# Optimization experiments

Measured on AMD Instinct MI355X. Metric: run time of the kernel, lower is better.

## Reference

```python
import jax, jax.numpy as jnp
import numpy as np

GRAD_CLIP = 50.0
MIN_DIST = 1e-10


def _logpsi(x_flat, W1, b1, W2, b2, w3):
    # x_flat: [D] flattened electron coordinates -> scalar log|psi|
    h = jnp.tanh(x_flat @ W1 + b1)
    h = jnp.tanh(h @ W2 + b2)
    return h @ w3


def setup_inputs() -> dict:
    key = jax.random.key(0)
    k = jax.random.split(key, 6)
    B, NE, H = 1024, 16, 512
    D = NE * 3
    electron_coords = jax.random.normal(k[0], (B, NE, 3), dtype=jnp.float32)
    atom_coords = jnp.asarray(
        [[0.0, 0.0, 0.0], [1.4, 0.0, 0.0], [0.0, 1.4, 0.0], [0.0, 0.0, 1.4]],
        dtype=jnp.float32)
    nuclear_charges = jnp.ones((4,), dtype=jnp.float32)
    W1 = jax.random.normal(k[1], (D, H), dtype=jnp.float32) / np.float32(np.sqrt(D))
    b1 = jnp.zeros((H,), dtype=jnp.float32)
    W2 = jax.random.normal(k[2], (H, H), dtype=jnp.float32) / np.float32(np.sqrt(H))
    b2 = jnp.zeros((H,), dtype=jnp.float32)
    w3 = jax.random.normal(k[3], (H,), dtype=jnp.float32) / np.float32(np.sqrt(H))
    return {"electron_coords": electron_coords, "atom_coords": atom_coords,
            "nuclear_charges": nuclear_charges,
            "W1": W1, "b1": b1, "W2": W2, "b2": b2, "w3": w3}


def _kinetic_log(electron_coords, W1, b1, W2, b2, w3):
    # kinetic = -0.5 * (lap log psi + |grad log psi|^2), per batch element
    B, NE, _ = electron_coords.shape
    D = NE * 3
    x = electron_coords.reshape(B, D)

    def f(xi):
        return _logpsi(xi, W1, b1, W2, b2, w3)

    def per_sample(xi):
        g = jax.grad(f)(xi)                       # [D]
        hdiag = jnp.diagonal(jax.jacfwd(jax.grad(f))(xi))  # [D]
        return g, hdiag

    g, hdiag = jax.vmap(per_sample)(x)            # [B, D] each
    hdiag = jnp.where(jnp.isfinite(hdiag),
                      jnp.clip(hdiag, -GRAD_CLIP, GRAD_CLIP), 0.0)
    lap = hdiag.sum(-1)
    gsq = (g ** 2).sum(-1)
    return jnp.clip(-0.5 * (lap + gsq), -100.0, 100.0)


def _potential(electron_coords, atom_coords, nuclear_charges):
    B, NE, _ = electron_coords.shape
    NA = atom_coords.shape[0]
    # electron-electron repulsion, sum over i<j
    d_ee = electron_coords[:, :, None, :] - electron_coords[:, None, :, :]
    r_ee = jnp.sqrt((d_ee ** 2).sum(-1) + jnp.eye(NE, dtype=electron_coords.dtype))
    r_ee = jnp.maximum(r_ee, MIN_DIST)
    iu = jnp.triu(jnp.ones((NE, NE), dtype=bool), 1)
    e_e = jnp.where(iu, 1.0 / r_ee, 0.0).sum((1, 2))
    # electron-nucleus attraction
    d_en = electron_coords[:, :, None, :] - atom_coords[None, None, :, :]
    r_en = jnp.maximum(jnp.sqrt((d_en ** 2).sum(-1)), MIN_DIST)  # [B, NE, NA]
    e_n = -(nuclear_charges[None, None, :] / r_en).sum((1, 2))
    # nucleus-nucleus repulsion (constant over batch)
    d_nn = atom_coords[:, None, :] - atom_coords[None, :, :]
    r_nn = jnp.sqrt((d_nn ** 2).sum(-1) + jnp.eye(NA, dtype=atom_coords.dtype))
    iun = jnp.triu(jnp.ones((NA, NA), dtype=bool), 1)
    zz = nuclear_charges[:, None] * nuclear_charges[None, :]
    n_n = jnp.where(iun & (r_nn > MIN_DIST), zz / r_nn, 0.0).sum()
    return jnp.clip(e_e + e_n + n_n, -1000.0, 1000.0)


def reference(electron_coords, atom_coords, nuclear_charges, W1, b1, W2, b2, w3):
    kinetic = _kinetic_log(electron_coords, W1, b1, W2, b2, w3)
    potential = _potential(electron_coords, atom_coords, nuclear_charges)
    return kinetic + potential
```

## Files before the change

kernel.cpp:

```cpp
#include <hip/hip_runtime.h>
#include <math.h>

#define BTOT 1024
#define NE   16
#define NA   4
#define DD   48
#define HH   512
#define ROWS (BTOT * DD)

#define GBM 128
#define GBN 128
#define GBK 64
#define NCB (HH / GBN)
#define MG  (NCB * (ROWS / GBM))
#define NU  128
#define NT  (HH / GBK)

typedef __attribute__((ext_vector_type(8))) short bf16x8;
typedef __attribute__((ext_vector_type(8))) unsigned short u16x8;
typedef __attribute__((ext_vector_type(4))) float f32x4;

__device__ inline unsigned short f2bf(float f) {
  unsigned int u = __builtin_bit_cast(unsigned int, f);
  u += 0x7fffu + ((u >> 16) & 1u);
  return (unsigned short)(u >> 16);
}
__device__ inline float bf2f(unsigned short s) {
  unsigned int u = ((unsigned int)s) << 16;
  return __builtin_bit_cast(float, u);
}

__device__ inline int swz(int row, int chunk) {
  return (row << 6) + ((chunk ^ (row & 7)) << 3);
}

__device__ inline void gload16(const ushort* g, ushort* l) {
  __builtin_amdgcn_global_load_lds(
      (const __attribute__((address_space(1))) unsigned int*)g,
      (__attribute__((address_space(3))) unsigned int*)l, 16, 0, 0);
}

__device__ inline void gemm128_k_loop(const ushort* __restrict__ abase,
                                      const ushort* __restrict__ bbase,
                                      ushort* As, ushort* Bs,
                                      int w, int l, f32x4 acc[4][4]) {
  const int lrow = l >> 3;
  const int cg = (l & 7) ^ lrow;
  const ushort* __restrict__ ap = abase + (w * 32 + lrow) * HH + cg * 8;
  const ushort* __restrict__ bp = bbase + (w * 32 + lrow) * HH + cg * 8;
  const int wm = w >> 1, wn = w & 1;
  const int lr = l & 15, lg = l >> 4;

#pragma unroll
  for (int q = 0; q < 4; ++q) {
    gload16(ap + q * 8 * HH, As + (w * 4 + q) * 512);
    gload16(bp + q * 8 * HH, Bs + (w * 4 + q) * 512);
  }
  __syncthreads();

  for (int kt = 0; kt < NT; ++kt) {
    const int cur = (kt & 1) << 13;
    if (kt + 1 < NT) {
      const int nxt = ((kt + 1) & 1) << 13;
      const int koff = (kt + 1) * GBK;
#pragma unroll
      for (int q = 0; q < 4; ++q) {
        gload16(ap + koff + q * 8 * HH, As + nxt + (w * 4 + q) * 512);
        gload16(bp + koff + q * 8 * HH, Bs + nxt + (w * 4 + q) * 512);
      }
    }
#pragma unroll
    for (int k0 = 0; k0 < GBK; k0 += 32) {
      const int ck = (k0 >> 3) + lg;
      bf16x8 af[4], bfr[4];
#pragma unroll
      for (int m = 0; m < 4; ++m)
        af[m] = *reinterpret_cast<const bf16x8*>(
            &As[cur + swz(wm * 64 + m * 16 + lr, ck)]);
#pragma unroll
      for (int n = 0; n < 4; ++n)
        bfr[n] = *reinterpret_cast<const bf16x8*>(
            &Bs[cur + swz(wn * 64 + n * 16 + lr, ck)]);
#pragma unroll
      for (int m = 0; m < 4; ++m)
#pragma unroll
        for (int n = 0; n < 4; ++n)
          acc[m][n] = __builtin_amdgcn_mfma_f32_16x16x32_bf16(af[m], bfr[n],
                                                              acc[m][n], 0, 0, 0);
    }
    __syncthreads();
  }
}

__device__ inline void gemm64_k_loop(const ushort* __restrict__ abase,
                                     const ushort* __restrict__ bbase,
                                     ushort* As, ushort* Bs,
                                     int w, int l, f32x4 acc[2][2]) {
  const int lrow = l >> 3;
  const int cg = (l & 7) ^ lrow;
  const ushort* __restrict__ ap = abase + (w * 16 + lrow) * HH + cg * 8;
  const ushort* __restrict__ bp = bbase + (w * 16 + lrow) * HH + cg * 8;
  const int wm = w >> 1, wn = w & 1;
  const int lr = l & 15, lg = l >> 4;

#pragma unroll
  for (int q = 0; q < 2; ++q) {
    gload16(ap + q * 8 * HH, As + (w * 2 + q) * 512);
    gload16(bp + q * 8 * HH, Bs + (w * 2 + q) * 512);
  }
  __syncthreads();

  for (int kt = 0; kt < NT; ++kt) {
    const int cur = (kt & 1) << 12;
    if (kt + 1 < NT) {
      const int nxt = ((kt + 1) & 1) << 12;
      const int koff = (kt + 1) * GBK;
#pragma unroll
      for (int q = 0; q < 2; ++q) {
        gload16(ap + koff + q * 8 * HH, As + nxt + (w * 2 + q) * 512);
        gload16(bp + koff + q * 8 * HH, Bs + nxt + (w * 2 + q) * 512);
      }
    }
#pragma unroll
    for (int k0 = 0; k0 < GBK; k0 += 32) {
      const int ck = (k0 >> 3) + lg;
      bf16x8 af[2], bfr[2];
#pragma unroll
      for (int m = 0; m < 2; ++m)
        af[m] = *reinterpret_cast<const bf16x8*>(
            &As[cur + swz(wm * 32 + m * 16 + lr, ck)]);
#pragma unroll
      for (int n = 0; n < 2; ++n)
        bfr[n] = *reinterpret_cast<const bf16x8*>(
            &Bs[cur + swz(wn * 32 + n * 16 + lr, ck)]);
#pragma unroll
      for (int m = 0; m < 2; ++m)
#pragma unroll
        for (int n = 0; n < 2; ++n)
          acc[m][n] = __builtin_amdgcn_mfma_f32_16x16x32_bf16(af[m], bfr[n],
                                                              acc[m][n], 0, 0, 0);
    }
    __syncthreads();
  }
}

__global__ __launch_bounds__(256) void k_l1pot(
    const float* __restrict__ X, const float* __restrict__ ATOM,
    const float* __restrict__ Z, const float* __restrict__ W1,
    const float* __restrict__ B1, const float* __restrict__ W2,
    ushort* __restrict__ W2b, ushort* __restrict__ W2Tb,
    ushort* __restrict__ T1b, float* __restrict__ D1,
    ushort* __restrict__ Ab, float* __restrict__ POT) {
  const int b = blockIdx.x, tid = threadIdx.x;
  __shared__ float xs[DD];
  __shared__ float d1s[HH];
  __shared__ float red[256];
  __shared__ float tile[32][33];

  if (b < 256) {
    const int bx = (b & 15) * 32, by = (b >> 4) * 32;
    const int tx = tid & 31, ty = tid >> 5;
    for (int r = 0; r < 32; r += 8) {
      float v = W2[(by + ty + r) * HH + bx + tx];
      tile[ty + r][tx] = v;
      W2b[(by + ty + r) * HH + bx + tx] = f2bf(v);
    }
    __syncthreads();
    for (int r = 0; r < 32; r += 8)
      W2Tb[(bx + ty + r) * HH + by + tx] = f2bf(tile[tx][ty + r]);
  }

  if (tid < DD) xs[tid] = X[b * DD + tid];
  __syncthreads();

  {
    const int j0 = tid * 2;
    float acc0 = B1[j0], acc1 = B1[j0 + 1];
#pragma unroll 8
    for (int i = 0; i < DD; ++i) {
      float xv = xs[i];
      float2 w = *reinterpret_cast<const float2*>(&W1[i * HH + j0]);
      acc0 = fmaf(xv, w.x, acc0);
      acc1 = fmaf(xv, w.y, acc1);
    }
    float t0 = tanhf(acc0), t1v = tanhf(acc1);
    unsigned int pk = ((unsigned int)f2bf(t1v) << 16) | f2bf(t0);
    *reinterpret_cast<unsigned int*>(&T1b[b * HH + j0]) = pk;
    float dd0 = 1.f - t0 * t0, dd1 = 1.f - t1v * t1v;
    d1s[j0] = dd0; d1s[j0 + 1] = dd1;
    *reinterpret_cast<float2*>(&D1[b * HH + j0]) = make_float2(dd0, dd1);
  }
  __syncthreads();

  {
    const int k0 = tid * 2;
    const float dd0 = d1s[k0], dd1 = d1s[k0 + 1];
#pragma unroll 4
    for (int i = 0; i < DD; ++i) {
      float2 w = *reinterpret_cast<const float2*>(&W1[i * HH + k0]);
      unsigned int pk =
          ((unsigned int)f2bf(w.y * dd1) << 16) | f2bf(w.x * dd0);
      *reinterpret_cast<unsigned int*>(&Ab[(b * DD + i) * HH + k0]) = pk;
    }
  }

  {
    float p = 0.f;
    for (int pr = tid; pr < NE * (NE - 1) / 2; pr += 256) {
      int i = 0, rem = pr;
      while (rem >= NE - 1 - i) { rem -= NE - 1 - i; ++i; }
      int j = i + 1 + rem;
      float dx = xs[i * 3 + 0] - xs[j * 3 + 0];
      float dy = xs[i * 3 + 1] - xs[j * 3 + 1];
      float dz = xs[i * 3 + 2] - xs[j * 3 + 2];
      float r = fmaxf(sqrtf(dx * dx + dy * dy + dz * dz), 1e-10f);
      p += 1.f / r;
    }
    for (int idx = tid; idx < NE * NA; idx += 256) {
      int e = idx / NA, a = idx % NA;
      float dx = xs[e * 3 + 0] - ATOM[a * 3 + 0];
      float dy = xs[e * 3 + 1] - ATOM[a * 3 + 1];
      float dz = xs[e * 3 + 2] - ATOM[a * 3 + 2];
      float r = fmaxf(sqrtf(dx * dx + dy * dy + dz * dz), 1e-10f);
      p -= Z[a] / r;
    }
    if (tid == 0) {
      for (int a = 0; a < NA; ++a)
        for (int a2 = a + 1; a2 < NA; ++a2) {
          float dx = ATOM[a * 3 + 0] - ATOM[a2 * 3 + 0];
          float dy = ATOM[a * 3 + 1] - ATOM[a2 * 3 + 1];
          float dz = ATOM[a * 3 + 2] - ATOM[a2 * 3 + 2];
          float r = sqrtf(dx * dx + dy * dy + dz * dz);
          if (r > 1e-10f) p += Z[a] * Z[a2] / r;
        }
    }
    red[tid] = p;
    __syncthreads();
    for (int s = 128; s > 0; s >>= 1) {
      if (tid < s) red[tid] += red[tid + s];
      __syncthreads();
    }
    if (tid == 0) POT[b] = fminf(fmaxf(red[0], -1000.f), 1000.f);
  }
}

__global__ __launch_bounds__(256) void k_act64(
    const ushort* __restrict__ Ab, const ushort* __restrict__ Bb,
    const float* __restrict__ B2, const float* __restrict__ w3,
    float* __restrict__ C2, ushort* __restrict__ Vb) {
  const int rb = blockIdx.x >> 3;
  const int cb = blockIdx.x & 7;
  const int row0 = rb * 64, col0 = cb * 64;
  const int t = threadIdx.x, w = t >> 6, l = t & 63;

  __shared__ ushort As[2 * 64 * GBK];
  __shared__ ushort Bs[2 * 64 * GBK];

  f32x4 acc[2][2];
#pragma unroll
  for (int m = 0; m < 2; ++m)
#pragma unroll
    for (int n = 0; n < 2; ++n) acc[m][n] = (f32x4)0.f;

  gemm64_k_loop(Ab + row0 * HH, Bb + col0 * HH, As, Bs, w, l, acc);

  const int wm = w >> 1, wn = w & 1, lr = l & 15, lg = l >> 4;
#pragma unroll
  for (int m = 0; m < 2; ++m)
#pragma unroll
    for (int e = 0; e < 4; ++e) {
      const int row = row0 + wm * 32 + m * 16 + lg * 4 + e;
#pragma unroll
      for (int n = 0; n < 2; ++n) {
        const int col = col0 + wn * 32 + n * 16 + lr;
        float a2 = acc[m][n][e] + B2[col];
        float t2 = tanhf(a2);
        float d2 = 1.f - t2 * t2;
        float w3v = w3[col];
        C2[row * HH + col] = -2.f * t2 * d2 * w3v;
        Vb[row * HH + col] = f2bf(w3v * d2);
      }
    }
}

__global__ __launch_bounds__(256) void k_mu(
    const ushort* __restrict__ Abig, const ushort* __restrict__ W2Tb,
    const float* __restrict__ C2, float* __restrict__ HD2P,
    const ushort* __restrict__ Vb, const ushort* __restrict__ W2b,
    const float* __restrict__ D1, const ushort* __restrict__ T1b,
    float* __restrict__ S1, ushort* __restrict__ C1b) {
  const int t = threadIdx.x, w = t >> 6, l = t & 63;
  __shared__ ushort As[2 * GBM * GBK];
  __shared__ ushort Bs[2 * GBN * GBK];

  if (blockIdx.x < NU) {
    const int ub = blockIdx.x;
    const int rb = ub >> 3, cb = ub & 7;
    const int row0 = rb * 64, col0 = cb * 64;

    f32x4 acc[2][2];
#pragma unroll
    for (int m = 0; m < 2; ++m)
#pragma unroll
      for (int n = 0; n < 2; ++n) acc[m][n] = (f32x4)0.f;

    gemm64_k_loop(Vb + row0 * HH, W2b + col0 * HH, As, Bs, w, l, acc);

    const int wm = w >> 1, wn = w & 1, lr = l & 15, lg = l >> 4;
#pragma unroll
    for (int m = 0; m < 2; ++m)
#pragma unroll
      for (int e = 0; e < 4; ++e) {
        const int row = row0 + wm * 32 + m * 16 + lg * 4 + e;
#pragma unroll
        for (int n = 0; n < 2; ++n) {
          const int col = col0 + wn * 32 + n * 16 + lr;
          float u = acc[m][n][e];
          float d1 = D1[row * HH + col];
          float t1 = bf2f(T1b[row * HH + col]);
          S1[row * HH + col] = d1 * u;
          C1b[row * HH + col] = f2bf(-2.f * t1 * d1 * u);
        }
      }
  } else {
    const int bid = blockIdx.x - NU;
    const int wgid = (bid & 7) * (MG / 8) + (bid >> 3);
    const int cb = wgid & 3;
    const int rb = wgid >> 2;
    const int row0 = rb * GBM, col0 = cb * GBN;

    f32x4 acc[4][4];
#pragma unroll
    for (int m = 0; m < 4; ++m)
#pragma unroll
      for (int n = 0; n < 4; ++n) acc[m][n] = (f32x4)0.f;

    gemm128_k_loop(Abig + row0 * HH, W2Tb + col0 * HH, As, Bs, w, l, acc);

    const int wm = w >> 1, wn = w & 1, lr = l & 15, lg = l >> 4;
#pragma unroll
    for (int m = 0; m < 4; ++m) {
#pragma unroll
      for (int e = 0; e < 4; ++e) {
        const int row_g = row0 + wm * 64 + m * 16 + lg * 4 + e;
        const int bs2 = row_g / DD;
        const float* __restrict__ c2p = &C2[bs2 * HH + col0 + wn * 64 + lr];
        float s = 0.f;
#pragma unroll
        for (int n = 0; n < 4; ++n) {
          float mv = acc[m][n][e];
          s = fmaf(c2p[n * 16] * mv, mv, s);
        }
        s += __shfl_xor(s, 1);
        s += __shfl_xor(s, 2);
        s += __shfl_xor(s, 4);
        s += __shfl_xor(s, 8);
        if (lr == 0) HD2P[cb * ROWS + row_g] = s;
      }
    }
  }
}

__global__ __launch_bounds__(256) void k_grad_fin(
    const float* __restrict__ W1, const float* __restrict__ S1,
    const ushort* __restrict__ C1b, const float* __restrict__ HD2P,
    const float* __restrict__ POT, float* __restrict__ OUT) {
  const int b = blockIdx.x, tid = threadIdx.x;
  __shared__ float gtmp[DD], htmp[DD];
  const int wid = tid >> 6, lane = tid & 63;
  const int j0 = lane * 8;

  for (int i = wid; i < DD; i += 4) {
    float4 wa = *reinterpret_cast<const float4*>(&W1[i * HH + j0]);
    float4 wb = *reinterpret_cast<const float4*>(&W1[i * HH + j0 + 4]);
    float4 sa = *reinterpret_cast<const float4*>(&S1[b * HH + j0]);
    float4 sb = *reinterpret_cast<const float4*>(&S1[b * HH + j0 + 4]);
    u16x8 cv = *reinterpret_cast<const u16x8*>(&C1b[b * HH + j0]);
    float wv[8] = {wa.x, wa.y, wa.z, wa.w, wb.x, wb.y, wb.z, wb.w};
    float sv[8] = {sa.x, sa.y, sa.z, sa.w, sb.x, sb.y, sb.z, sb.w};
    float gp = 0.f, hp = 0.f;
#pragma unroll
    for (int e = 0; e < 8; ++e) {
      gp = fmaf(wv[e], sv[e], gp);
      hp = fmaf(wv[e] * wv[e], bf2f(cv[e]), hp);
    }
#pragma unroll
    for (int off = 32; off > 0; off >>= 1) {
      gp += __shfl_down(gp, off);
      hp += __shfl_down(hp, off);
    }
    if (lane == 0) { gtmp[i] = gp; htmp[i] = hp; }
  }
  __syncthreads();

  if (tid < 64) {
    float gv = 0.f, hv = 0.f;
    if (tid < DD) {
      gv = gtmp[tid];
      float h = htmp[tid];
#pragma unroll
      for (int c = 0; c < NCB; ++c) h += HD2P[c * ROWS + b * DD + tid];
      if (h >= -1e30f && h <= 1e30f) h = fminf(fmaxf(h, -50.f), 50.f);
      else h = 0.f;
      hv = h;
    }
    float sq = gv * gv;
#pragma unroll
    for (int off = 32; off > 0; off >>= 1) {
      sq += __shfl_down(sq, off);
      hv += __shfl_down(hv, off);
    }
    if (tid == 0) {
      float kin = fminf(fmaxf(-0.5f * (hv + sq), -100.f), 100.f);
      OUT[b] = kin + POT[b];
    }
  }
}

extern "C" void kernel_launch(void* const* d_in, const int* in_sizes, int n_in,
                              void* d_out, int out_size, void* d_ws, size_t ws_size,
                              hipStream_t stream) {
  const float* X    = (const float*)d_in[0];
  const float* ATOM = (const float*)d_in[1];
  const float* Z    = (const float*)d_in[2];
  const float* W1   = (const float*)d_in[3];
  const float* B1   = (const float*)d_in[4];
  const float* W2   = (const float*)d_in[5];
  const float* B2   = (const float*)d_in[6];
  const float* w3   = (const float*)d_in[7];
  float* out = (float*)d_out;

  float* ws = (float*)d_ws;
  ushort* W2b  = (ushort*)(ws + 0);
  ushort* W2Tb = (ushort*)(ws + 131072);
  ushort* T1b  = (ushort*)(ws + 262144);
  ushort* Vb   = (ushort*)(ws + 524288);
  ushort* C1b  = (ushort*)(ws + 786432);
  float*  S1   = ws + 1048576;
  float*  D1   = ws + 1572864;
  float*  C2   = ws + 2097152;
  float*  POT  = ws + 2621440;
  float*  HD2P = ws + 2622464;
  ushort* Abig = (ushort*)(ws + 2819072);

  k_l1pot<<<BTOT, 256, 0, stream>>>(X, ATOM, Z, W1, B1, W2, W2b, W2Tb,
                                    T1b, D1, Abig, POT);
  k_act64<<<128, 256, 0, stream>>>(T1b, W2Tb, B2, w3, C2, Vb);
  k_mu<<<NU + MG, 256, 0, stream>>>(Abig, W2Tb, C2, HD2P,
                                    Vb, W2b, D1, T1b, S1, C1b);
  k_grad_fin<<<BTOT, 256, 0, stream>>>(W1, S1, C1b, HD2P, POT, out);
}
```

Measured before the change: 101.4 us.

## Enlarge k_mu big GEMM tile to 256x128 with 512-thread blocks

```diff
diff --git a/kernel.cpp b/kernel.cpp
--- a/kernel.cpp
+++ b/kernel.cpp
@@ -8,13 +8,13 @@
 #define HH   512
 #define ROWS (BTOT * DD)
 
-#define GBM 128
-#define GBN 128
-#define GBK 64
-#define NCB (HH / GBN)
-#define MG  (NCB * (ROWS / GBM))
-#define NU  128
-#define NT  (HH / GBK)
+#define GBM2 256
+#define GBN  128
+#define GBK  64
+#define NCB  (HH / GBN)
+#define MG2  (NCB * (ROWS / GBM2))
+#define NU   128
+#define NT   (HH / GBK)
 
 typedef __attribute__((ext_vector_type(8))) short bf16x8;
 typedef __attribute__((ext_vector_type(8))) unsigned short u16x8;
@@ -38,58 +38,6 @@
   __builtin_amdgcn_global_load_lds(
       (const __attribute__((address_space(1))) unsigned int*)g,
       (__attribute__((address_space(3))) unsigned int*)l, 16, 0, 0);
-}
-
-__device__ inline void gemm128_k_loop(const ushort* __restrict__ abase,
-                                      const ushort* __restrict__ bbase,
-                                      ushort* As, ushort* Bs,
-                                      int w, int l, f32x4 acc[4][4]) {
-  const int lrow = l >> 3;
-  const int cg = (l & 7) ^ lrow;
-  const ushort* __restrict__ ap = abase + (w * 32 + lrow) * HH + cg * 8;
-  const ushort* __restrict__ bp = bbase + (w * 32 + lrow) * HH + cg * 8;
-  const int wm = w >> 1, wn = w & 1;
-  const int lr = l & 15, lg = l >> 4;
-
-#pragma unroll
-  for (int q = 0; q < 4; ++q) {
-    gload16(ap + q * 8 * HH, As + (w * 4 + q) * 512);
-    gload16(bp + q * 8 * HH, Bs + (w * 4 + q) * 512);
-  }
-  __syncthreads();
-
-  for (int kt = 0; kt < NT; ++kt) {
-    const int cur = (kt & 1) << 13;
-    if (kt + 1 < NT) {
-      const int nxt = ((kt + 1) & 1) << 13;
-      const int koff = (kt + 1) * GBK;
-#pragma unroll
-      for (int q = 0; q < 4; ++q) {
-        gload16(ap + koff + q * 8 * HH, As + nxt + (w * 4 + q) * 512);
-        gload16(bp + koff + q * 8 * HH, Bs + nxt + (w * 4 + q) * 512);
-      }
-    }
-#pragma unroll
-    for (int k0 = 0; k0 < GBK; k0 += 32) {
-      const int ck = (k0 >> 3) + lg;
-      bf16x8 af[4], bfr[4];
-#pragma unroll
-      for (int m = 0; m < 4; ++m)
-        af[m] = *reinterpret_cast<const bf16x8*>(
-            &As[cur + swz(wm * 64 + m * 16 + lr, ck)]);
-#pragma unroll
-      for (int n = 0; n < 4; ++n)
-        bfr[n] = *reinterpret_cast<const bf16x8*>(
-            &Bs[cur + swz(wn * 64 + n * 16 + lr, ck)]);
-#pragma unroll
-      for (int m = 0; m < 4; ++m)
-#pragma unroll
-        for (int n = 0; n < 4; ++n)
-          acc[m][n] = __builtin_amdgcn_mfma_f32_16x16x32_bf16(af[m], bfr[n],
-                                                              acc[m][n], 0, 0, 0);
-    }
-    __syncthreads();
-  }
 }
 
 __device__ inline void gemm64_k_loop(const ushort* __restrict__ abase,
@@ -283,51 +231,79 @@
     }
 }
 
-__global__ __launch_bounds__(256) void k_mu(
+__global__ __launch_bounds__(512) void k_mu(
     const ushort* __restrict__ Abig, const ushort* __restrict__ W2Tb,
     const float* __restrict__ C2, float* __restrict__ HD2P,
     const ushort* __restrict__ Vb, const ushort* __restrict__ W2b,
     const float* __restrict__ D1, const ushort* __restrict__ T1b,
     float* __restrict__ S1, ushort* __restrict__ C1b) {
   const int t = threadIdx.x, w = t >> 6, l = t & 63;
-  __shared__ ushort As[2 * GBM * GBK];
+  __shared__ ushort As[2 * GBM2 * GBK];
   __shared__ ushort Bs[2 * GBN * GBK];
+
+  const int lrow = l >> 3;
+  const int cg = (l & 7) ^ lrow;
+  const int lr = l & 15, lg = l >> 4;
 
   if (blockIdx.x < NU) {
     const int ub = blockIdx.x;
     const int rb = ub >> 3, cb = ub & 7;
     const int row0 = rb * 64, col0 = cb * 64;
-
-    f32x4 acc[2][2];
-#pragma unroll
-    for (int m = 0; m < 2; ++m)
-#pragma unroll
-      for (int n = 0; n < 2; ++n) acc[m][n] = (f32x4)0.f;
-
-    gemm64_k_loop(Vb + row0 * HH, W2b + col0 * HH, As, Bs, w, l, acc);
-
-    const int wm = w >> 1, wn = w & 1, lr = l & 15, lg = l >> 4;
+    const ushort* __restrict__ ap = Vb  + (row0 + w * 8 + lrow) * HH + cg * 8;
+    const ushort* __restrict__ bp = W2b + (col0 + w * 8 + lrow) * HH + cg * 8;
+    const int wm = w >> 2, wn = w & 3;
+
+    f32x4 acc[2];
+    acc[0] = (f32x4)0.f; acc[1] = (f32x4)0.f;
+
+    gload16(ap, As + w * 512);
+    gload16(bp, Bs + w * 512);
+    __syncthreads();
+
+    for (int kt = 0; kt < NT; ++kt) {
+      const int curA = (kt & 1) << 14, curB = (kt & 1) << 13;
+      if (kt + 1 < NT) {
+        const int nA = ((kt + 1) & 1) << 14, nB = ((kt + 1) & 1) << 13;
+        const int koff = (kt + 1) * GBK;
+        gload16(ap + koff, As + nA + w * 512);
+        gload16(bp + koff, Bs + nB + w * 512);
+      }
+#pragma unroll
+      for (int k0 = 0; k0 < GBK; k0 += 32) {
+        const int ck = (k0 >> 3) + lg;
+        bf16x8 af0 = *reinterpret_cast<const bf16x8*>(
+            &As[curA + swz(wm * 32 + lr, ck)]);
+        bf16x8 af1 = *reinterpret_cast<const bf16x8*>(
+            &As[curA + swz(wm * 32 + 16 + lr, ck)]);
+        bf16x8 bf = *reinterpret_cast<const bf16x8*>(
+            &Bs[curB + swz(wn * 16 + lr, ck)]);
+        acc[0] = __builtin_amdgcn_mfma_f32_16x16x32_bf16(af0, bf, acc[0], 0, 0, 0);
+        acc[1] = __builtin_amdgcn_mfma_f32_16x16x32_bf16(af1, bf, acc[1], 0, 0, 0);
+      }
+      __syncthreads();
+    }
+
 #pragma unroll
     for (int m = 0; m < 2; ++m)
 #pragma unroll
       for (int e = 0; e < 4; ++e) {
         const int row = row0 + wm * 32 + m * 16 + lg * 4 + e;
-#pragma unroll
-        for (int n = 0; n < 2; ++n) {
-          const int col = col0 + wn * 32 + n * 16 + lr;
-          float u = acc[m][n][e];
-          float d1 = D1[row * HH + col];
-          float t1 = bf2f(T1b[row * HH + col]);
-          S1[row * HH + col] = d1 * u;
-          C1b[row * HH + col] = f2bf(-2.f * t1 * d1 * u);
-        }
+        const int col = col0 + wn * 16 + lr;
+        float u = acc[m][e];
+        float d1 = D1[row * HH + col];
+        float t1 = bf2f(T1b[row * HH + col]);
+        S1[row * HH + col] = d1 * u;
+        C1b[row * HH + col] = f2bf(-2.f * t1 * d1 * u);
       }
   } else {
     const int bid = blockIdx.x - NU;
-    const int wgid = (bid & 7) * (MG / 8) + (bid >> 3);
+    const int wgid = (bid & 7) * (MG2 / 8) + (bid >> 3);
     const int cb = wgid & 3;
     const int rb = wgid >> 2;
-    const int row0 = rb * GBM, col0 = cb * GBN;
+    const int row0 = rb * GBM2, col0 = cb * GBN;
+    const ushort* __restrict__ ap = Abig + (row0 + w * 32 + lrow) * HH + cg * 8;
+    const ushort* __restrict__ bp = W2Tb + (col0 + w * 16 + lrow) * HH + cg * 8;
+    const int wm = w >> 1, wn = w & 1;
 
     f32x4 acc[4][4];
 #pragma unroll
@@ -335,9 +311,48 @@
 #pragma unroll
       for (int n = 0; n < 4; ++n) acc[m][n] = (f32x4)0.f;
 
-    gemm128_k_loop(Abig + row0 * HH, W2Tb + col0 * HH, As, Bs, w, l, acc);
-
-    const int wm = w >> 1, wn = w & 1, lr = l & 15, lg = l >> 4;
+#pragma unroll
+    for (int q = 0; q < 4; ++q)
+      gload16(ap + q * 8 * HH, As + (w * 4 + q) * 512);
+#pragma unroll
+    for (int q = 0; q < 2; ++q)
+      gload16(bp + q * 8 * HH, Bs + (w * 2 + q) * 512);
+    __syncthreads();
+
+    for (int kt = 0; kt < NT; ++kt) {
+      const int curA = (kt & 1) << 14, curB = (kt & 1) << 13;
+      if (kt + 1 < NT) {
+        const int nA = ((kt + 1) & 1) << 14, nB = ((kt + 1) & 1) << 13;
+        const int koff = (kt + 1) * GBK;
+#pragma unroll
+        for (int q = 0; q < 4; ++q)
+          gload16(ap + koff + q * 8 * HH, As + nA + (w * 4 + q) * 512);
+#pragma unroll
+        for (int q = 0; q < 2; ++q)
+          gload16(bp + koff + q * 8 * HH, Bs + nB + (w * 2 + q) * 512);
+      }
+#pragma unroll
+      for (int k0 = 0; k0 < GBK; k0 += 32) {
+        const int ck = (k0 >> 3) + lg;
+        bf16x8 af[4], bfr[4];
+#pragma unroll
+        for (int m = 0; m < 4; ++m)
+          af[m] = *reinterpret_cast<const bf16x8*>(
+              &As[curA + swz(wm * 64 + m * 16 + lr, ck)]);
+#pragma unroll
+        for (int n = 0; n < 4; ++n)
+          bfr[n] = *reinterpret_cast<const bf16x8*>(
+              &Bs[curB + swz(wn * 64 + n * 16 + lr, ck)]);
+#pragma unroll
+        for (int m = 0; m < 4; ++m)
+#pragma unroll
+          for (int n = 0; n < 4; ++n)
+            acc[m][n] = __builtin_amdgcn_mfma_f32_16x16x32_bf16(af[m], bfr[n],
+                                                                acc[m][n], 0, 0, 0);
+      }
+      __syncthreads();
+    }
+
 #pragma unroll
     for (int m = 0; m < 4; ++m) {
 #pragma unroll
@@ -446,7 +461,7 @@
   k_l1pot<<<BTOT, 256, 0, stream>>>(X, ATOM, Z, W1, B1, W2, W2b, W2Tb,
                                     T1b, D1, Abig, POT);
   k_act64<<<128, 256, 0, stream>>>(T1b, W2Tb, B2, w3, C2, Vb);
-  k_mu<<<NU + MG, 256, 0, stream>>>(Abig, W2Tb, C2, HD2P,
-                                    Vb, W2b, D1, T1b, S1, C1b);
+  k_mu<<<NU + MG2, 512, 0, stream>>>(Abig, W2Tb, C2, HD2P,
+                                     Vb, W2b, D1, T1b, S1, C1b);
   k_grad_fin<<<BTOT, 256, 0, stream>>>(W1, S1, C1b, HD2P, POT, out);
 }
```

Measured after the change: 99.31 us. -2.1%, faster.
